# Kernel optimization log

Measured on AMD Instinct MI355X. Metric: run time of the kernel, lower is better.

The kernel has to match this reference:

```python
import jax, jax.numpy as jnp
import numpy as np

V, D, NH, L, E, TOPK, S, B = 512, 768, 12, 4, 8, 2, 1024, 4
DH = int(2.0 * D)  # d_hidden_mult * d_model
DHEAD = D // NH


def setup_inputs() -> dict:
    key = jax.random.key(0)
    ks = jax.random.split(key, 10)
    def n(k, shape):
        return jax.random.normal(k, shape, jnp.float32) * 0.02
    return {
        "x": jax.random.randint(ks[0], (B, S), 0, V),
        "tok_emb": n(ks[1], (V, D)),           # tied with LM head
        "pos_emb": n(ks[2], (1, S, D)),
        "ln1_g": jnp.ones((L, D)), "ln1_b": jnp.zeros((L, D)),
        "qkv_w": n(ks[3], (L, D, 3 * D)), "qkv_b": jnp.zeros((L, 3 * D)),
        "proj_w": n(ks[4], (L, D, D)), "proj_b": jnp.zeros((L, D)),
        "ln2_g": jnp.ones((L, D)), "ln2_b": jnp.zeros((L, D)),
        "gate_w": n(ks[5], (L, D, E)), "gate_b": jnp.zeros((L, E)),
        "w1": n(ks[6], (L, E, D, DH)), "b1": jnp.zeros((L, E, DH)),
        "w2": n(ks[7], (L, E, DH, D)), "b2": jnp.zeros((L, E, D)),
        "lnf_g": jnp.ones((D,)), "lnf_b": jnp.zeros((D,)),
    }


def _layernorm(x, g, b, eps=1e-5):
    m = jnp.mean(x, -1, keepdims=True)
    v = jnp.var(x, -1, keepdims=True)
    return (x - m) / jnp.sqrt(v + eps) * g + b


def _attn(x, qkv_w, qkv_b, proj_w, proj_b):
    b, t, d = x.shape
    qkv = (x @ qkv_w + qkv_b).reshape(b, t, 3, NH, DHEAD)
    qkv = jnp.transpose(qkv, (2, 0, 3, 1, 4))  # [3,B,H,T,dh]
    q, k, v = qkv[0], qkv[1], qkv[2]
    scores = jnp.einsum("bhqd,bhkd->bhqk", q, k) / jnp.sqrt(jnp.float32(DHEAD))
    causal = jnp.tril(jnp.ones((t, t), bool))
    scores = jnp.where(causal[None, None], scores, jnp.finfo(scores.dtype).min)
    attn = jax.nn.softmax(scores, axis=-1)
    out = jnp.einsum("bhqk,bhkd->bhqd", attn, v)
    out = jnp.transpose(out, (0, 2, 1, 3)).reshape(b, t, d)
    return out @ proj_w + proj_b


def _moe(x, gate_w, gate_b, w1, b1, w2, b2):
    b, t, d = x.shape
    xt = x.reshape(-1, d)                                    # [N,D]
    gl = xt @ gate_w + gate_b                                # [N,E]
    probs = jax.nn.softmax(gl, axis=-1)
    topv, topi = jax.lax.top_k(probs, TOPK)                  # [N,K]
    topv = topv / jnp.sum(topv, -1, keepdims=True)           # renormalize top-k
    nidx = jnp.arange(xt.shape[0])[:, None]
    combine = jnp.zeros((xt.shape[0], E), xt.dtype).at[nidx, topi].set(topv)
    h = jax.nn.gelu(jnp.einsum("nd,edh->neh", xt, w1) + b1)  # [N,E,DH]
    eo = jnp.einsum("neh,ehd->ned", h, w2) + b2              # [N,E,D]
    y = jnp.einsum("ne,ned->nd", combine, eo)
    return y.reshape(b, t, d)


def reference(x, tok_emb, pos_emb, ln1_g, ln1_b, qkv_w, qkv_b, proj_w, proj_b,
              ln2_g, ln2_b, gate_w, gate_b, w1, b1, w2, b2, lnf_g, lnf_b):
    h = tok_emb[x] + pos_emb[:, : x.shape[1], :]
    for i in range(L):
        h = h + _attn(_layernorm(h, ln1_g[i], ln1_b[i]), qkv_w[i], qkv_b[i], proj_w[i], proj_b[i])
        h = h + _moe(_layernorm(h, ln2_g[i], ln2_b[i]), gate_w[i], gate_b[i], w1[i], b1[i], w2[i], b2[i])
    h = _layernorm(h, lnf_g, lnf_b)
    logits = h @ tok_emb.T  # tied LM head
    return logits
```

## Files before the change

### kernel.cpp

```cpp
#include <hip/hip_runtime.h>
#include <cstdint>
#include <cstddef>

#define SEQ 1024
#define DMODEL 768
#define NHEAD 12
#define DHEAD 64
#define NLAYER 4
#define NEXP 8
#define DHID 1536
#define VOCAB 512
#define NTOK 4096

typedef __attribute__((ext_vector_type(4))) float f32x4;
typedef __attribute__((ext_vector_type(8))) unsigned short us8v;
typedef __attribute__((ext_vector_type(4))) unsigned short us4v;
typedef __attribute__((ext_vector_type(8))) __bf16 bf16x8;
union FragU { us8v u; bf16x8 b; };

__global__ __launch_bounds__(256) void embed_kernel(const int* __restrict__ x,
    const float* __restrict__ tok, const float* __restrict__ pos, float* __restrict__ h) {
  int i = blockIdx.x * 256 + threadIdx.x;
  int n = i / DMODEL, d = i - n * DMODEL;
  int s = n & (SEQ - 1);
  h[i] = tok[(size_t)x[n] * DMODEL + d] + pos[(size_t)s * DMODEL + d];
}

__global__ __launch_bounds__(256) void ln_kernel(const float* __restrict__ x,
    const float* __restrict__ g, const float* __restrict__ b, float* __restrict__ y) {
  int row = blockIdx.x;
  const float* xr = x + (size_t)row * DMODEL;
  int t = threadIdx.x;
  float v0 = xr[t], v1 = xr[t + 256], v2 = xr[t + 512];
  float s = v0 + v1 + v2;
  float s2 = v0 * v0 + v1 * v1 + v2 * v2;
  for (int off = 32; off; off >>= 1) { s += __shfl_down(s, off); s2 += __shfl_down(s2, off); }
  __shared__ float rs[4], rq[4];
  if ((t & 63) == 0) { rs[t >> 6] = s; rq[t >> 6] = s2; }
  __syncthreads();
  float S  = rs[0] + rs[1] + rs[2] + rs[3];
  float S2 = rq[0] + rq[1] + rq[2] + rq[3];
  float m = S * (1.f / DMODEL);
  float var = S2 * (1.f / DMODEL) - m * m;
  float r = rsqrtf(var + 1e-5f);
  float* yr = y + (size_t)row * DMODEL;
  yr[t]       = (v0 - m) * r * g[t]       + b[t];
  yr[t + 256] = (v1 - m) * r * g[t + 256] + b[t + 256];
  yr[t + 512] = (v2 - m) * r * g[t + 512] + b[t + 512];
}

#define BM 128
#define BN 128
#define BK 32

__device__ __forceinline__ int chx(int row, int kb) {
  return row * 32 + ((kb ^ ((row >> 1) & 3)) << 3);
}

__device__ __forceinline__ void cvt8(const f32x4 x0, const f32x4 x1, us8v& h, us8v& l) {
#pragma unroll
  for (int j = 0; j < 4; j++) {
    unsigned int bb = __float_as_uint(x0[j]);
    h[j] = (unsigned short)(bb >> 16);
    float fl = x0[j] - __uint_as_float(bb & 0xffff0000u);
    l[j] = (unsigned short)(__float_as_uint(fl) >> 16);
  }
#pragma unroll
  for (int j = 0; j < 4; j++) {
    unsigned int bb = __float_as_uint(x1[j]);
    h[4 + j] = (unsigned short)(bb >> 16);
    float fl = x1[j] - __uint_as_float(bb & 0xffff0000u);
    l[4 + j] = (unsigned short)(__float_as_uint(fl) >> 16);
  }
}

template<bool TRANSB, bool RESID>
__global__ __launch_bounds__(256, 2) void gemm_mfma(
    const float* __restrict__ A, const float* __restrict__ Bm,
    const float* __restrict__ bias, float* __restrict__ C,
    int M, int Nn, int K)
{
  __shared__ __align__(16) unsigned short AsH[BM * 32], AsL[BM * 32];
  __shared__ __align__(16) unsigned short BsH[BN * 32], BsL[BN * 32];
  int bm = blockIdx.y * BM, bn = blockIdx.x * BN;
  int tid = threadIdx.x;
  int lane = tid & 63;
  int wid = tid >> 6;
  int wr = wid >> 1, wc = wid & 1;
  int frow = lane & 15, fkb = lane >> 4;
  f32x4 zero = {0.f, 0.f, 0.f, 0.f};
  f32x4 acc[4][4];
#pragma unroll
  for (int i = 0; i < 4; i++)
#pragma unroll
    for (int j = 0; j < 4; j++) acc[i][j] = zero;

  int sr = tid & 127;
  bool doB = tid >= 128;

  for (int k0 = 0; k0 < K; k0 += BK) {
    if (!doB) {
      const float* Ap = A + (size_t)(bm + sr) * K + k0;
#pragma unroll
      for (int c = 0; c < 4; c++) {
        f32x4 x0 = *(const f32x4*)(Ap + c * 8);
        f32x4 x1 = *(const f32x4*)(Ap + c * 8 + 4);
        us8v h, l; cvt8(x0, x1, h, l);
        *(us8v*)&AsH[chx(sr, c)] = h;
        *(us8v*)&AsL[chx(sr, c)] = l;
      }
    } else if (TRANSB) {
      const float* Bp = Bm + (size_t)(bn + sr) * K + k0;
#pragma unroll
      for (int c = 0; c < 4; c++) {
        f32x4 x0 = *(const f32x4*)(Bp + c * 8);
        f32x4 x1 = *(const f32x4*)(Bp + c * 8 + 4);
        us8v h, l; cvt8(x0, x1, h, l);
        *(us8v*)&BsH[chx(sr, c)] = h;
        *(us8v*)&BsL[chx(sr, c)] = l;
      }
    } else {
      const float* Bp = Bm + (size_t)k0 * Nn + bn + sr;
#pragma unroll
      for (int c = 0; c < 4; c++) {
        f32x4 x0, x1;
#pragma unroll
        for (int j = 0; j < 4; j++) x0[j] = Bp[(size_t)(c * 8 + j) * Nn];
#pragma unroll
        for (int j = 0; j < 4; j++) x1[j] = Bp[(size_t)(c * 8 + 4 + j) * Nn];
        us8v h, l; cvt8(x0, x1, h, l);
        *(us8v*)&BsH[chx(sr, c)] = h;
        *(us8v*)&BsL[chx(sr, c)] = l;
      }
    }
    __syncthreads();
    FragU ah[4], al[4], bh[4], bl[4];
#pragma unroll
    for (int i = 0; i < 4; i++) {
      ah[i].u = *(const us8v*)&AsH[chx(wr * 64 + i * 16 + frow, fkb)];
      al[i].u = *(const us8v*)&AsL[chx(wr * 64 + i * 16 + frow, fkb)];
      bh[i].u = *(const us8v*)&BsH[chx(wc * 64 + i * 16 + frow, fkb)];
      bl[i].u = *(const us8v*)&BsL[chx(wc * 64 + i * 16 + frow, fkb)];
    }
#pragma unroll
    for (int i = 0; i < 4; i++)
#pragma unroll
      for (int j = 0; j < 4; j++)
        acc[i][j] = __builtin_amdgcn_mfma_f32_16x16x32_bf16(ah[i].b, bh[j].b, acc[i][j], 0, 0, 0);
#pragma unroll
    for (int i = 0; i < 4; i++)
#pragma unroll
      for (int j = 0; j < 4; j++)
        acc[i][j] = __builtin_amdgcn_mfma_f32_16x16x32_bf16(ah[i].b, bl[j].b, acc[i][j], 0, 0, 0);
#pragma unroll
    for (int i = 0; i < 4; i++)
#pragma unroll
      for (int j = 0; j < 4; j++)
        acc[i][j] = __builtin_amdgcn_mfma_f32_16x16x32_bf16(al[i].b, bh[j].b, acc[i][j], 0, 0, 0);
    __syncthreads();
  }
#pragma unroll
  for (int i = 0; i < 4; i++) {
    int rbase = bm + wr * 64 + i * 16 + (lane >> 4) * 4;
#pragma unroll
    for (int q = 0; q < 4; q++) {
      float* Crow = C + (size_t)(rbase + q) * Nn;
#pragma unroll
      for (int j = 0; j < 4; j++) {
        int col = bn + wc * 64 + j * 16 + frow;
        float v = acc[i][j][q] + (bias ? bias[col] : 0.f);
        if (RESID) v += Crow[col];
        Crow[col] = v;
      }
    }
  }
}

__device__ __forceinline__ float gelu_f(float x) {
  float x3 = x * x * x;
  return 0.5f * x * (1.f + tanhf(0.7978845608028654f * (x + 0.044715f * x3)));
}

template<bool GELU, bool SCALE>
__global__ __launch_bounds__(256, 2) void gemm_moe_mfma(
    const float* __restrict__ A, const float* __restrict__ Bbase,
    const float* __restrict__ biasBase, float* __restrict__ C,
    const int* __restrict__ entries, const int* __restrict__ counts,
    const float* __restrict__ tokw, int Nn, int K)
{
  int e = blockIdx.z;
  int cnt = counts[e];
  int bm = blockIdx.y * BM;
  if (bm >= cnt) return;
  const float* Bm = Bbase + (size_t)e * K * Nn;
  const float* bias = biasBase + (size_t)e * Nn;
  const int* list = entries + e * NTOK;
  int bn = blockIdx.x * BN;
  int tid = threadIdx.x;
  int lane = tid & 63;
  int wid = tid >> 6;
  int wr = wid >> 1, wc = wid & 1;
  int frow = lane & 15, fkb = lane >> 4;

  __shared__ __align__(16) unsigned short AsH[BM * 32], AsL[BM * 32];
  __shared__ __align__(16) unsigned short BsH[BN * 32], BsL[BN * 32];
  __shared__ int rowent[BM];
  if (tid < BM) {
    int gr = bm + tid;
    rowent[tid] = (gr < cnt) ? list[gr] : -1;
  }
  __syncthreads();

  f32x4 zero = {0.f, 0.f, 0.f, 0.f};
  f32x4 acc[4][4];
#pragma unroll
  for (int i = 0; i < 4; i++)
#pragma unroll
    for (int j = 0; j < 4; j++) acc[i][j] = zero;

  int sr = tid & 127;
  bool doB = tid >= 128;

  for (int k0 = 0; k0 < K; k0 += BK) {
    if (!doB) {
      int ent = rowent[sr];
      if (ent >= 0) {
        int arow = GELU ? (ent >> 1) : ent;
        const float* Ap = A + (size_t)arow * K + k0;
#pragma unroll
        for (int c = 0; c < 4; c++) {
          f32x4 x0 = *(const f32x4*)(Ap + c * 8);
          f32x4 x1 = *(const f32x4*)(Ap + c * 8 + 4);
          us8v h, l; cvt8(x0, x1, h, l);
          *(us8v*)&AsH[chx(sr, c)] = h;
          *(us8v*)&AsL[chx(sr, c)] = l;
        }
      } else {
        us8v z = {0, 0, 0, 0, 0, 0, 0, 0};
#pragma unroll
        for (int c = 0; c < 4; c++) {
          *(us8v*)&AsH[chx(sr, c)] = z;
          *(us8v*)&AsL[chx(sr, c)] = z;
        }
      }
    } else {
      const float* Bp = Bm + (size_t)k0 * Nn + bn + sr;
#pragma unroll
      for (int c = 0; c < 4; c++) {
        f32x4 x0, x1;
#pragma unroll
        for (int j = 0; j < 4; j++) x0[j] = Bp[(size_t)(c * 8 + j) * Nn];
#pragma unroll
        for (int j = 0; j < 4; j++) x1[j] = Bp[(size_t)(c * 8 + 4 + j) * Nn];
        us8v h, l; cvt8(x0, x1, h, l);
        *(us8v*)&BsH[chx(sr, c)] = h;
        *(us8v*)&BsL[chx(sr, c)] = l;
      }
    }
    __syncthreads();
    FragU ah[4], al[4], bh[4], bl[4];
#pragma unroll
    for (int i = 0; i < 4; i++) {
      ah[i].u = *(const us8v*)&AsH[chx(wr * 64 + i * 16 + frow, fkb)];
      al[i].u = *(const us8v*)&AsL[chx(wr * 64 + i * 16 + frow, fkb)];
      bh[i].u = *(const us8v*)&BsH[chx(wc * 64 + i * 16 + frow, fkb)];
      bl[i].u = *(const us8v*)&BsL[chx(wc * 64 + i * 16 + frow, fkb)];
    }
#pragma unroll
    for (int i = 0; i < 4; i++)
#pragma unroll
      for (int j = 0; j < 4; j++)
        acc[i][j] = __builtin_amdgcn_mfma_f32_16x16x32_bf16(ah[i].b, bh[j].b, acc[i][j], 0, 0, 0);
#pragma unroll
    for (int i = 0; i < 4; i++)
#pragma unroll
      for (int j = 0; j < 4; j++)
        acc[i][j] = __builtin_amdgcn_mfma_f32_16x16x32_bf16(ah[i].b, bl[j].b, acc[i][j], 0, 0, 0);
#pragma unroll
    for (int i = 0; i < 4; i++)
#pragma unroll
      for (int j = 0; j < 4; j++)
        acc[i][j] = __builtin_amdgcn_mfma_f32_16x16x32_bf16(al[i].b, bh[j].b, acc[i][j], 0, 0, 0);
    __syncthreads();
  }
#pragma unroll
  for (int i = 0; i < 4; i++) {
    int rloc = wr * 64 + i * 16 + (lane >> 4) * 4;
#pragma unroll
    for (int q = 0; q < 4; q++) {
      int ent = rowent[rloc + q];
      if (ent < 0) continue;
      float scl = SCALE ? tokw[ent] : 1.f;
      float* Crow = C + (size_t)ent * Nn;
#pragma unroll
      for (int j = 0; j < 4; j++) {
        int col = bn + wc * 64 + j * 16 + frow;
        float v = acc[i][j][q] + bias[col];
        if (GELU) v = gelu_f(v);
        if (SCALE) v *= scl;
        Crow[col] = v;
      }
    }
  }
}

__device__ __forceinline__ int kvx(int row, int col) {
  return (row << 6) + (((((col >> 3) ^ (row & 7))) << 3) | (col & 7));
}

__global__ __launch_bounds__(256, 2) void fattn_mfma(const float* __restrict__ qkv,
                                                     float* __restrict__ out) {
  int qt = blockIdx.x;
  int hh = blockIdx.y;
  int b  = blockIdx.z;
  int n0 = b * SEQ;
  int q0 = qt * 64;
  const float* base = qkv + (size_t)n0 * (3 * DMODEL);
  int tid = threadIdx.x;
  int lane = tid & 63;
  int w = tid >> 6;
  int fr = lane & 15, fg = lane >> 4;

  __shared__ __align__(16) unsigned short KsH[64 * 64], KsL[64 * 64];
  __shared__ float Vs[64][64];
  __shared__ float Psf[4][16][68];

  FragU qh[2], ql[2];
  {
    const float* qrow = base + (size_t)(q0 + w * 16 + fr) * (3 * DMODEL) + hh * DHEAD;
#pragma unroll
    for (int s = 0; s < 2; s++) {
      f32x4 x0 = *(const f32x4*)(qrow + s * 32 + fg * 8);
      f32x4 x1 = *(const f32x4*)(qrow + s * 32 + fg * 8 + 4);
      x0 *= 0.125f; x1 *= 0.125f;
      cvt8(x0, x1, qh[s].u, ql[s].u);
    }
  }

  f32x4 O[4];
  float m_i[4], l_i[4];
#pragma unroll
  for (int c = 0; c < 4; c++) O[c] = (f32x4){0.f, 0.f, 0.f, 0.f};
#pragma unroll
  for (int r = 0; r < 4; r++) { m_i[r] = -3.4e38f; l_i[r] = 0.f; }

  int krow = tid >> 2, kd = (tid & 3) << 4;

  for (int kt = 0; kt <= qt; kt++) {
    int k0 = kt * 64;
    __syncthreads();
    {
      const float* kp = base + (size_t)(k0 + krow) * (3 * DMODEL) + DMODEL + hh * DHEAD + kd;
      f32x4 x0 = *(const f32x4*)(kp);
      f32x4 x1 = *(const f32x4*)(kp + 4);
      f32x4 x2 = *(const f32x4*)(kp + 8);
      f32x4 x3 = *(const f32x4*)(kp + 12);
      us8v h0, l0, h1, l1;
      cvt8(x0, x1, h0, l0); cvt8(x2, x3, h1, l1);
      *(us8v*)&KsH[kvx(krow, kd)]     = h0;
      *(us8v*)&KsH[kvx(krow, kd + 8)] = h1;
      *(us8v*)&KsL[kvx(krow, kd)]     = l0;
      *(us8v*)&KsL[kvx(krow, kd + 8)] = l1;
    }
    {
#pragma unroll
      for (int it = 0; it < 16; it++) {
        int i = tid + it * 256;
        int r = i >> 6, c = i & 63;
        Vs[r][c] = base[(size_t)(k0 + r) * (3 * DMODEL) + 2 * DMODEL + hh * DHEAD + c];
      }
    }
    __syncthreads();

    f32x4 sa[4];
#pragma unroll
    for (int f = 0; f < 4; f++) sa[f] = (f32x4){0.f, 0.f, 0.f, 0.f};
#pragma unroll
    for (int s = 0; s < 2; s++) {
#pragma unroll
      for (int f = 0; f < 4; f++) {
        FragU kh, kl;
        kh.u = *(const us8v*)&KsH[kvx(f * 16 + fr, s * 32 + fg * 8)];
        kl.u = *(const us8v*)&KsL[kvx(f * 16 + fr, s * 32 + fg * 8)];
        sa[f] = __builtin_amdgcn_mfma_f32_16x16x32_bf16(qh[s].b, kh.b, sa[f], 0, 0, 0);
        sa[f] = __builtin_amdgcn_mfma_f32_16x16x32_bf16(qh[s].b, kl.b, sa[f], 0, 0, 0);
        sa[f] = __builtin_amdgcn_mfma_f32_16x16x32_bf16(ql[s].b, kh.b, sa[f], 0, 0, 0);
      }
    }
    if (kt == qt) {
#pragma unroll
      for (int f = 0; f < 4; f++)
#pragma unroll
        for (int r = 0; r < 4; r++)
          if (k0 + f * 16 + fr > q0 + w * 16 + fg * 4 + r) sa[f][r] = -3.4e38f;
    }

#pragma unroll
    for (int r = 0; r < 4; r++) {
      float rm = fmaxf(fmaxf(sa[0][r], sa[1][r]), fmaxf(sa[2][r], sa[3][r]));
      rm = fmaxf(rm, __shfl_xor(rm, 1));
      rm = fmaxf(rm, __shfl_xor(rm, 2));
      rm = fmaxf(rm, __shfl_xor(rm, 4));
      rm = fmaxf(rm, __shfl_xor(rm, 8));
      float mnew = fmaxf(m_i[r], rm);
      float alpha = __expf(m_i[r] - mnew);
      m_i[r] = mnew;
      float rsum = 0.f;
#pragma unroll
      for (int f = 0; f < 4; f++) {
        float p = __expf(sa[f][r] - mnew);
        rsum += p;
        Psf[w][fg * 4 + r][f * 16 + fr] = p;
      }
      rsum += __shfl_xor(rsum, 1);
      rsum += __shfl_xor(rsum, 2);
      rsum += __shfl_xor(rsum, 4);
      rsum += __shfl_xor(rsum, 8);
      l_i[r] = l_i[r] * alpha + rsum;
#pragma unroll
      for (int c = 0; c < 4; c++) O[c][r] *= alpha;
    }
    __syncthreads();

    for (int kk = 0; kk < 64; kk++) {
      float pr[4], vv[4];
#pragma unroll
      for (int r = 0; r < 4; r++) pr[r] = Psf[w][fg * 4 + r][kk];
#pragma unroll
      for (int c = 0; c < 4; c++) vv[c] = Vs[kk][c * 16 + fr];
#pragma unroll
      for (int c = 0; c < 4; c++)
#pragma unroll
        for (int r = 0; r < 4; r++) O[c][r] += pr[r] * vv[c];
    }
  }

#pragma unroll
  for (int r = 0; r < 4; r++) {
    float rinv = 1.f / l_i[r];
    float* orow = out + (size_t)(n0 + q0 + w * 16 + fg * 4 + r) * DMODEL + hh * DHEAD;
#pragma unroll
    for (int c = 0; c < 4; c++) orow[c * 16 + fr] = O[c][r] * rinv;
  }
}

__global__ __launch_bounds__(256) void gate_kernel(const float* __restrict__ xln,
    const float* __restrict__ gw, const float* __restrict__ gb,
    int* __restrict__ counts, int* __restrict__ entries, float* __restrict__ tokw) {
  int n = blockIdx.x * 256 + threadIdx.x;
  if (n >= NTOK) return;
  const float* xr = xln + (size_t)n * DMODEL;
  float gl[NEXP];
#pragma unroll
  for (int e = 0; e < NEXP; e++) gl[e] = gb[e];
  for (int dd = 0; dd < DMODEL; dd++) {
    float xv = xr[dd];
#pragma unroll
    for (int e = 0; e < NEXP; e++) gl[e] += xv * gw[dd * NEXP + e];
  }
  float mx = gl[0];
#pragma unroll
  for (int e = 1; e < NEXP; e++) mx = fmaxf(mx, gl[e]);
  float ex[NEXP];
#pragma unroll
  for (int e = 0; e < NEXP; e++) ex[e] = expf(gl[e] - mx);
  int i0 = 0; float v0 = ex[0];
#pragma unroll
  for (int e = 1; e < NEXP; e++) if (ex[e] > v0) { v0 = ex[e]; i0 = e; }
  int i1 = -1; float v1 = -1.f;
#pragma unroll
  for (int e = 0; e < NEXP; e++) if (e != i0 && ex[e] > v1) { v1 = ex[e]; i1 = e; }
  float wsum = v0 + v1;
  float w0 = v0 / wsum, w1 = v1 / wsum;
  int p0 = atomicAdd(&counts[i0], 1);
  entries[i0 * NTOK + p0] = n * 2 + 0;
  tokw[n * 2 + 0] = w0;
  int p1 = atomicAdd(&counts[i1], 1);
  entries[i1 * NTOK + p1] = n * 2 + 1;
  tokw[n * 2 + 1] = w1;
}

__global__ void zero_counts(int* c) { if (threadIdx.x < NEXP) c[threadIdx.x] = 0; }

__global__ __launch_bounds__(256) void combine_kernel(float* __restrict__ h,
                                                      const float* __restrict__ eo) {
  int i = blockIdx.x * 256 + threadIdx.x;
  int n = i / DMODEL, d = i - n * DMODEL;
  h[i] += eo[(size_t)(n * 2) * DMODEL + d] + eo[(size_t)(n * 2 + 1) * DMODEL + d];
}

extern "C" void kernel_launch(void* const* d_in, const int* in_sizes, int n_in,
                              void* d_out, int out_size, void* d_ws, size_t ws_size,
                              hipStream_t stream) {
  const int*   x       = (const int*)d_in[0];
  const float* tok_emb = (const float*)d_in[1];
  const float* pos_emb = (const float*)d_in[2];
  const float* ln1_g   = (const float*)d_in[3];
  const float* ln1_b   = (const float*)d_in[4];
  const float* qkv_w   = (const float*)d_in[5];
  const float* qkv_b   = (const float*)d_in[6];
  const float* proj_w  = (const float*)d_in[7];
  const float* proj_b  = (const float*)d_in[8];
  const float* ln2_g   = (const float*)d_in[9];
  const float* ln2_b   = (const float*)d_in[10];
  const float* gate_w  = (const float*)d_in[11];
  const float* gate_b  = (const float*)d_in[12];
  const float* w1      = (const float*)d_in[13];
  const float* b1      = (const float*)d_in[14];
  const float* w2      = (const float*)d_in[15];
  const float* b2      = (const float*)d_in[16];
  const float* lnf_g   = (const float*)d_in[17];
  const float* lnf_b   = (const float*)d_in[18];
  float* out = (float*)d_out;

  const size_t ND = (size_t)NTOK * DMODEL;
  float* h    = (float*)d_ws;
  float* xln  = h + ND;
  float* R    = xln + ND;
  float* R2   = R + (size_t)2 * NTOK * DHID;
  float* tokw = R2 + (size_t)2 * NTOK * DMODEL;
  int* counts  = (int*)(tokw + 2 * NTOK);
  int* entries = counts + NEXP;

  float* qkvbuf   = R;
  float* H1       = R;
  float* attn_out = R2;
  float* eo       = R2;

  dim3 blk(256);
  embed_kernel<<<ND / 256, blk, 0, stream>>>(x, tok_emb, pos_emb, h);
  for (int l = 0; l < NLAYER; l++) {
    ln_kernel<<<NTOK, blk, 0, stream>>>(h, ln1_g + l * DMODEL, ln1_b + l * DMODEL, xln);
    gemm_mfma<false, false><<<dim3(3 * DMODEL / BN, NTOK / BM), blk, 0, stream>>>(
        xln, qkv_w + (size_t)l * DMODEL * 3 * DMODEL, qkv_b + l * 3 * DMODEL,
        qkvbuf, NTOK, 3 * DMODEL, DMODEL);
    fattn_mfma<<<dim3(SEQ / 64, NHEAD, 4), blk, 0, stream>>>(qkvbuf, attn_out);
    gemm_mfma<false, true><<<dim3(DMODEL / BN, NTOK / BM), blk, 0, stream>>>(
        attn_out, proj_w + (size_t)l * DMODEL * DMODEL, proj_b + l * DMODEL,
        h, NTOK, DMODEL, DMODEL);
    ln_kernel<<<NTOK, blk, 0, stream>>>(h, ln2_g + l * DMODEL, ln2_b + l * DMODEL, xln);
    zero_counts<<<1, 64, 0, stream>>>(counts);
    gate_kernel<<<NTOK / 256, blk, 0, stream>>>(
        xln, gate_w + (size_t)l * DMODEL * NEXP, gate_b + l * NEXP, counts, entries, tokw);
    gemm_moe_mfma<true, false><<<dim3(DHID / BN, NTOK / BM, NEXP), blk, 0, stream>>>(
        xln, w1 + (size_t)l * NEXP * DMODEL * DHID, b1 + (size_t)l * NEXP * DHID,
        H1, entries, counts, tokw, DHID, DMODEL);
    gemm_moe_mfma<false, true><<<dim3(DMODEL / BN, NTOK / BM, NEXP), blk, 0, stream>>>(
        H1, w2 + (size_t)l * NEXP * DHID * DMODEL, b2 + (size_t)l * NEXP * DMODEL,
        eo, entries, counts, tokw, DMODEL, DHID);
    combine_kernel<<<ND / 256, blk, 0, stream>>>(h, eo);
  }
  ln_kernel<<<NTOK, blk, 0, stream>>>(h, lnf_g, lnf_b, xln);
  gemm_mfma<true, false><<<dim3(VOCAB / BN, NTOK / BM), blk, 0, stream>>>(
      xln, tok_emb, nullptr, out, NTOK, VOCAB, DMODEL);
}
```

Baseline: 3.374 ms.

## Pre-split operands into bf16 hi/lo planes and transpose weights before GEMMs

Weights are converted once per layer into transposed bf16 hi/lo arrays by a new split-transpose kernel. Activations are emitted already split by layernorm, attention and the first MoE GEMM. The GEMM inner loops then copy ready-made u16 data instead of loading fp32, splitting, and doing strided column reads of untransposed B. This removes redundant conversion work and uncoalesced B loads, at the cost of extra per-call weight preprocessing passes and a larger workspace.

```diff
diff --git a/kernel.cpp b/kernel.cpp
--- a/kernel.cpp
+++ b/kernel.cpp
@@ -17,6 +17,27 @@
 typedef __attribute__((ext_vector_type(4))) unsigned short us4v;
 typedef __attribute__((ext_vector_type(8))) __bf16 bf16x8;
 union FragU { us8v u; bf16x8 b; };
+typedef unsigned short u16;
+
+__device__ __forceinline__ void split1(float x, u16& h, u16& l) {
+  unsigned int u = __float_as_uint(x);
+  h = (u16)(u >> 16);
+  float fl = x - __uint_as_float(u & 0xffff0000u);
+  l = (u16)(__float_as_uint(fl) >> 16);
+}
+
+__device__ __forceinline__ void cvt8(const f32x4 x0, const f32x4 x1, us8v& h, us8v& l) {
+#pragma unroll
+  for (int j = 0; j < 4; j++) { u16 hh, ll; split1(x0[j], hh, ll); h[j] = hh; l[j] = ll; }
+#pragma unroll
+  for (int j = 0; j < 4; j++) { u16 hh, ll; split1(x1[j], hh, ll); h[4 + j] = hh; l[4 + j] = ll; }
+}
+
+__device__ __forceinline__ void cvt4(float a, float b, float c, float d, us4v& h, us4v& l) {
+  float x[4] = {a, b, c, d};
+#pragma unroll
+  for (int j = 0; j < 4; j++) { u16 hh, ll; split1(x[j], hh, ll); h[j] = hh; l[j] = ll; }
+}
 
 __global__ __launch_bounds__(256) void embed_kernel(const int* __restrict__ x,
     const float* __restrict__ tok, const float* __restrict__ pos, float* __restrict__ h) {
@@ -27,7 +48,8 @@
 }
 
 __global__ __launch_bounds__(256) void ln_kernel(const float* __restrict__ x,
-    const float* __restrict__ g, const float* __restrict__ b, float* __restrict__ y) {
+    const float* __restrict__ g, const float* __restrict__ b, float* __restrict__ y,
+    u16* __restrict__ yh, u16* __restrict__ yl) {
   int row = blockIdx.x;
   const float* xr = x + (size_t)row * DMODEL;
   int t = threadIdx.x;
@@ -43,10 +65,56 @@
   float m = S * (1.f / DMODEL);
   float var = S2 * (1.f / DMODEL) - m * m;
   float r = rsqrtf(var + 1e-5f);
-  float* yr = y + (size_t)row * DMODEL;
-  yr[t]       = (v0 - m) * r * g[t]       + b[t];
-  yr[t + 256] = (v1 - m) * r * g[t + 256] + b[t + 256];
-  yr[t + 512] = (v2 - m) * r * g[t + 512] + b[t + 512];
+  size_t base = (size_t)row * DMODEL;
+#pragma unroll
+  for (int q = 0; q < 3; q++) {
+    int idx = t + q * 256;
+    float v = (q == 0 ? v0 : (q == 1 ? v1 : v2));
+    float o = (v - m) * r * g[idx] + b[idx];
+    y[base + idx] = o;
+    u16 hh, ll; split1(o, hh, ll);
+    yh[base + idx] = hh; yl[base + idx] = ll;
+  }
+}
+
+__global__ __launch_bounds__(256) void split_tr_kernel(const float* __restrict__ src,
+    u16* __restrict__ dh, u16* __restrict__ dl, int K, int N) {
+  size_t slab = (size_t)blockIdx.z * K * N;
+  src += slab; dh += slab; dl += slab;
+  int n0 = blockIdx.x * 64, k0 = blockIdx.y * 64;
+  __shared__ u16 Th[64][72], Tl[64][72];
+  int t = threadIdx.x;
+  int vk = (t >> 4) * 4;
+  int vn = (t & 15) * 4;
+  const float* sp = src + (size_t)(k0 + vk) * N + n0 + vn;
+  f32x4 r0 = *(const f32x4*)(sp);
+  f32x4 r1 = *(const f32x4*)(sp + N);
+  f32x4 r2 = *(const f32x4*)(sp + 2 * N);
+  f32x4 r3 = *(const f32x4*)(sp + 3 * N);
+#pragma unroll
+  for (int j = 0; j < 4; j++) {
+    us4v hh, ll;
+    cvt4(r0[j], r1[j], r2[j], r3[j], hh, ll);
+    *(us4v*)&Th[vn + j][vk] = hh;
+    *(us4v*)&Tl[vn + j][vk] = ll;
+  }
+  __syncthreads();
+  int nr = t >> 2, kc = (t & 3) * 16;
+  u16* dhp = dh + (size_t)(n0 + nr) * K + k0 + kc;
+  u16* dlp = dl + (size_t)(n0 + nr) * K + k0 + kc;
+  *(us8v*)dhp       = *(const us8v*)&Th[nr][kc];
+  *(us8v*)(dhp + 8) = *(const us8v*)&Th[nr][kc + 8];
+  *(us8v*)dlp       = *(const us8v*)&Tl[nr][kc];
+  *(us8v*)(dlp + 8) = *(const us8v*)&Tl[nr][kc + 8];
+}
+
+__global__ __launch_bounds__(256) void split_copy_kernel(const float* __restrict__ src,
+    u16* __restrict__ dh, u16* __restrict__ dl) {
+  int i = (blockIdx.x * 256 + threadIdx.x) * 8;
+  f32x4 x0 = *(const f32x4*)(src + i);
+  f32x4 x1 = *(const f32x4*)(src + i + 4);
+  us8v h, l; cvt8(x0, x1, h, l);
+  *(us8v*)&dh[i] = h; *(us8v*)&dl[i] = l;
 }
 
 #define BM 128
@@ -57,31 +125,15 @@
   return row * 32 + ((kb ^ ((row >> 1) & 3)) << 3);
 }
 
-__device__ __forceinline__ void cvt8(const f32x4 x0, const f32x4 x1, us8v& h, us8v& l) {
-#pragma unroll
-  for (int j = 0; j < 4; j++) {
-    unsigned int bb = __float_as_uint(x0[j]);
-    h[j] = (unsigned short)(bb >> 16);
-    float fl = x0[j] - __uint_as_float(bb & 0xffff0000u);
-    l[j] = (unsigned short)(__float_as_uint(fl) >> 16);
-  }
-#pragma unroll
-  for (int j = 0; j < 4; j++) {
-    unsigned int bb = __float_as_uint(x1[j]);
-    h[4 + j] = (unsigned short)(bb >> 16);
-    float fl = x1[j] - __uint_as_float(bb & 0xffff0000u);
-    l[4 + j] = (unsigned short)(__float_as_uint(fl) >> 16);
-  }
-}
-
-template<bool TRANSB, bool RESID>
-__global__ __launch_bounds__(256, 2) void gemm_mfma(
-    const float* __restrict__ A, const float* __restrict__ Bm,
+template<bool RESID>
+__global__ __launch_bounds__(256, 2) void gemm_mfma_s(
+    const u16* __restrict__ Ah, const u16* __restrict__ Al,
+    const u16* __restrict__ Bh, const u16* __restrict__ Bl,
     const float* __restrict__ bias, float* __restrict__ C,
-    int M, int Nn, int K)
+    int Nn, int K)
 {
-  __shared__ __align__(16) unsigned short AsH[BM * 32], AsL[BM * 32];
-  __shared__ __align__(16) unsigned short BsH[BN * 32], BsL[BN * 32];
+  __shared__ __align__(16) u16 AsH[BM * 32], AsL[BM * 32];
+  __shared__ __align__(16) u16 BsH[BN * 32], BsL[BN * 32];
   int bm = blockIdx.y * BM, bn = blockIdx.x * BN;
   int tid = threadIdx.x;
   int lane = tid & 63;
@@ -100,37 +152,20 @@
 
   for (int k0 = 0; k0 < K; k0 += BK) {
     if (!doB) {
-      const float* Ap = A + (size_t)(bm + sr) * K + k0;
+      const u16* ph = Ah + (size_t)(bm + sr) * K + k0;
+      const u16* pl = Al + (size_t)(bm + sr) * K + k0;
 #pragma unroll
       for (int c = 0; c < 4; c++) {
-        f32x4 x0 = *(const f32x4*)(Ap + c * 8);
-        f32x4 x1 = *(const f32x4*)(Ap + c * 8 + 4);
-        us8v h, l; cvt8(x0, x1, h, l);
-        *(us8v*)&AsH[chx(sr, c)] = h;
-        *(us8v*)&AsL[chx(sr, c)] = l;
-      }
-    } else if (TRANSB) {
-      const float* Bp = Bm + (size_t)(bn + sr) * K + k0;
+        *(us8v*)&AsH[chx(sr, c)] = *(const us8v*)(ph + c * 8);
+        *(us8v*)&AsL[chx(sr, c)] = *(const us8v*)(pl + c * 8);
+      }
+    } else {
+      const u16* ph = Bh + (size_t)(bn + sr) * K + k0;
+      const u16* pl = Bl + (size_t)(bn + sr) * K + k0;
 #pragma unroll
       for (int c = 0; c < 4; c++) {
-        f32x4 x0 = *(const f32x4*)(Bp + c * 8);
-        f32x4 x1 = *(const f32x4*)(Bp + c * 8 + 4);
-        us8v h, l; cvt8(x0, x1, h, l);
-        *(us8v*)&BsH[chx(sr, c)] = h;
-        *(us8v*)&BsL[chx(sr, c)] = l;
-      }
-    } else {
-      const float* Bp = Bm + (size_t)k0 * Nn + bn + sr;
-#pragma unroll
-      for (int c = 0; c < 4; c++) {
-        f32x4 x0, x1;
-#pragma unroll
-        for (int j = 0; j < 4; j++) x0[j] = Bp[(size_t)(c * 8 + j) * Nn];
-#pragma unroll
-        for (int j = 0; j < 4; j++) x1[j] = Bp[(size_t)(c * 8 + 4 + j) * Nn];
-        us8v h, l; cvt8(x0, x1, h, l);
-        *(us8v*)&BsH[chx(sr, c)] = h;
-        *(us8v*)&BsL[chx(sr, c)] = l;
+        *(us8v*)&BsH[chx(sr, c)] = *(const us8v*)(ph + c * 8);
+        *(us8v*)&BsL[chx(sr, c)] = *(const us8v*)(pl + c * 8);
       }
     }
     __syncthreads();
@@ -181,10 +216,12 @@
   return 0.5f * x * (1.f + tanhf(0.7978845608028654f * (x + 0.044715f * x3)));
 }
 
-template<bool GELU, bool SCALE>
-__global__ __launch_bounds__(256, 2) void gemm_moe_mfma(
-    const float* __restrict__ A, const float* __restrict__ Bbase,
-    const float* __restrict__ biasBase, float* __restrict__ C,
+template<bool GELU>
+__global__ __launch_bounds__(256, 2) void gemm_moe_mfma_s(
+    const u16* __restrict__ Ah, const u16* __restrict__ Al,
+    const u16* __restrict__ Bh, const u16* __restrict__ Bl,
+    const float* __restrict__ biasBase,
+    float* __restrict__ Cf, u16* __restrict__ Ch, u16* __restrict__ Cl,
     const int* __restrict__ entries, const int* __restrict__ counts,
     const float* __restrict__ tokw, int Nn, int K)
 {
@@ -192,7 +229,8 @@
   int cnt = counts[e];
   int bm = blockIdx.y * BM;
   if (bm >= cnt) return;
-  const float* Bm = Bbase + (size_t)e * K * Nn;
+  const u16* Bph = Bh + (size_t)e * K * Nn;
+  const u16* Bpl = Bl + (size_t)e * K * Nn;
   const float* bias = biasBase + (size_t)e * Nn;
   const int* list = entries + e * NTOK;
   int bn = blockIdx.x * BN;
@@ -202,8 +240,8 @@
   int wr = wid >> 1, wc = wid & 1;
   int frow = lane & 15, fkb = lane >> 4;
 
-  __shared__ __align__(16) unsigned short AsH[BM * 32], AsL[BM * 32];
-  __shared__ __align__(16) unsigned short BsH[BN * 32], BsL[BN * 32];
+  __shared__ __align__(16) u16 AsH[BM * 32], AsL[BM * 32];
+  __shared__ __align__(16) u16 BsH[BN * 32], BsL[BN * 32];
   __shared__ int rowent[BM];
   if (tid < BM) {
     int gr = bm + tid;
@@ -226,14 +264,12 @@
       int ent = rowent[sr];
       if (ent >= 0) {
         int arow = GELU ? (ent >> 1) : ent;
-        const float* Ap = A + (size_t)arow * K + k0;
+        const u16* ph = Ah + (size_t)arow * K + k0;
+        const u16* pl = Al + (size_t)arow * K + k0;
 #pragma unroll
         for (int c = 0; c < 4; c++) {
-          f32x4 x0 = *(const f32x4*)(Ap + c * 8);
-          f32x4 x1 = *(const f32x4*)(Ap + c * 8 + 4);
-          us8v h, l; cvt8(x0, x1, h, l);
-          *(us8v*)&AsH[chx(sr, c)] = h;
-          *(us8v*)&AsL[chx(sr, c)] = l;
+          *(us8v*)&AsH[chx(sr, c)] = *(const us8v*)(ph + c * 8);
+          *(us8v*)&AsL[chx(sr, c)] = *(const us8v*)(pl + c * 8);
         }
       } else {
         us8v z = {0, 0, 0, 0, 0, 0, 0, 0};
@@ -244,17 +280,12 @@
         }
       }
     } else {
-      const float* Bp = Bm + (size_t)k0 * Nn + bn + sr;
+      const u16* ph = Bph + (size_t)(bn + sr) * K + k0;
+      const u16* pl = Bpl + (size_t)(bn + sr) * K + k0;
 #pragma unroll
       for (int c = 0; c < 4; c++) {
-        f32x4 x0, x1;
-#pragma unroll
-        for (int j = 0; j < 4; j++) x0[j] = Bp[(size_t)(c * 8 + j) * Nn];
-#pragma unroll
-        for (int j = 0; j < 4; j++) x1[j] = Bp[(size_t)(c * 8 + 4 + j) * Nn];
-        us8v h, l; cvt8(x0, x1, h, l);
-        *(us8v*)&BsH[chx(sr, c)] = h;
-        *(us8v*)&BsL[chx(sr, c)] = l;
+        *(us8v*)&BsH[chx(sr, c)] = *(const us8v*)(ph + c * 8);
+        *(us8v*)&BsL[chx(sr, c)] = *(const us8v*)(pl + c * 8);
       }
     }
     __syncthreads();
@@ -290,15 +321,18 @@
     for (int q = 0; q < 4; q++) {
       int ent = rowent[rloc + q];
       if (ent < 0) continue;
-      float scl = SCALE ? tokw[ent] : 1.f;
-      float* Crow = C + (size_t)ent * Nn;
 #pragma unroll
       for (int j = 0; j < 4; j++) {
         int col = bn + wc * 64 + j * 16 + frow;
         float v = acc[i][j][q] + bias[col];
-        if (GELU) v = gelu_f(v);
-        if (SCALE) v *= scl;
-        Crow[col] = v;
+        if (GELU) {
+          v = gelu_f(v);
+          u16 hh, ll; split1(v, hh, ll);
+          Ch[(size_t)ent * Nn + col] = hh;
+          Cl[(size_t)ent * Nn + col] = ll;
+        } else {
+          Cf[(size_t)ent * Nn + col] = v * tokw[ent];
+        }
       }
     }
   }
@@ -309,7 +343,8 @@
 }
 
 __global__ __launch_bounds__(256, 2) void fattn_mfma(const float* __restrict__ qkv,
-                                                     float* __restrict__ out) {
+                                                     u16* __restrict__ outh,
+                                                     u16* __restrict__ outl) {
   int qt = blockIdx.x;
   int hh = blockIdx.y;
   int b  = blockIdx.z;
@@ -321,7 +356,7 @@
   int w = tid >> 6;
   int fr = lane & 15, fg = lane >> 4;
 
-  __shared__ __align__(16) unsigned short KsH[64 * 64], KsL[64 * 64];
+  __shared__ __align__(16) u16 KsH[64 * 64], KsL[64 * 64];
   __shared__ float Vs[64][64];
   __shared__ float Psf[4][16][68];
 
@@ -438,9 +473,14 @@
 #pragma unroll
   for (int r = 0; r < 4; r++) {
     float rinv = 1.f / l_i[r];
-    float* orow = out + (size_t)(n0 + q0 + w * 16 + fg * 4 + r) * DMODEL + hh * DHEAD;
-#pragma unroll
-    for (int c = 0; c < 4; c++) orow[c * 16 + fr] = O[c][r] * rinv;
+    size_t obase = (size_t)(n0 + q0 + w * 16 + fg * 4 + r) * DMODEL + hh * DHEAD;
+#pragma unroll
+    for (int c = 0; c < 4; c++) {
+      float o = O[c][r] * rinv;
+      u16 hh2, ll2; split1(o, hh2, ll2);
+      outh[obase + c * 16 + fr] = hh2;
+      outl[obase + c * 16 + fr] = ll2;
+    }
   }
 }
 
@@ -514,43 +554,63 @@
   float* out = (float*)d_out;
 
   const size_t ND = (size_t)NTOK * DMODEL;
-  float* h    = (float*)d_ws;
-  float* xln  = h + ND;
-  float* R    = xln + ND;
-  float* R2   = R + (size_t)2 * NTOK * DHID;
-  float* tokw = R2 + (size_t)2 * NTOK * DMODEL;
-  int* counts  = (int*)(tokw + 2 * NTOK);
-  int* entries = counts + NEXP;
-
-  float* qkvbuf   = R;
-  float* H1       = R;
-  float* attn_out = R2;
-  float* eo       = R2;
+  char* W = (char*)d_ws;
+  float* h      = (float*)W;  W += ND * 4;
+  float* xln    = (float*)W;  W += ND * 4;
+  u16*   xh     = (u16*)W;    W += ND * 2;
+  u16*   xl     = (u16*)W;    W += ND * 2;
+  float* qkvbuf = (float*)W;  W += 3 * ND * 4;
+  u16*   aoh    = (u16*)W;    W += ND * 2;
+  u16*   aol    = (u16*)W;    W += ND * 2;
+  u16*   H1h    = (u16*)W;    W += (size_t)2 * NTOK * DHID * 2;
+  u16*   H1l    = (u16*)W;    W += (size_t)2 * NTOK * DHID * 2;
+  float* eo     = (float*)W;  W += (size_t)2 * NTOK * DMODEL * 4;
+  float* tokw   = (float*)W;  W += 2 * NTOK * 4;
+  int*   counts = (int*)W;    W += 32;
+  int*   entries= (int*)W;    W += (size_t)NEXP * NTOK * 4;
+  u16*   WTqh   = (u16*)W;    W += (size_t)DMODEL * 3 * DMODEL * 2;
+  u16*   WTql   = (u16*)W;    W += (size_t)DMODEL * 3 * DMODEL * 2;
+  u16*   WTph   = (u16*)W;    W += (size_t)DMODEL * DMODEL * 2;
+  u16*   WTpl   = (u16*)W;    W += (size_t)DMODEL * DMODEL * 2;
+  u16*   WT1h   = (u16*)W;    W += (size_t)NEXP * DMODEL * DHID * 2;
+  u16*   WT1l   = (u16*)W;    W += (size_t)NEXP * DMODEL * DHID * 2;
+  u16*   WT2h   = (u16*)W;    W += (size_t)NEXP * DHID * DMODEL * 2;
+  u16*   WT2l   = (u16*)W;    W += (size_t)NEXP * DHID * DMODEL * 2;
 
   dim3 blk(256);
   embed_kernel<<<ND / 256, blk, 0, stream>>>(x, tok_emb, pos_emb, h);
   for (int l = 0; l < NLAYER; l++) {
-    ln_kernel<<<NTOK, blk, 0, stream>>>(h, ln1_g + l * DMODEL, ln1_b + l * DMODEL, xln);
-    gemm_mfma<false, false><<<dim3(3 * DMODEL / BN, NTOK / BM), blk, 0, stream>>>(
-        xln, qkv_w + (size_t)l * DMODEL * 3 * DMODEL, qkv_b + l * 3 * DMODEL,
-        qkvbuf, NTOK, 3 * DMODEL, DMODEL);
-    fattn_mfma<<<dim3(SEQ / 64, NHEAD, 4), blk, 0, stream>>>(qkvbuf, attn_out);
-    gemm_mfma<false, true><<<dim3(DMODEL / BN, NTOK / BM), blk, 0, stream>>>(
-        attn_out, proj_w + (size_t)l * DMODEL * DMODEL, proj_b + l * DMODEL,
-        h, NTOK, DMODEL, DMODEL);
-    ln_kernel<<<NTOK, blk, 0, stream>>>(h, ln2_g + l * DMODEL, ln2_b + l * DMODEL, xln);
+    split_tr_kernel<<<dim3(3 * DMODEL / 64, DMODEL / 64, 1), blk, 0, stream>>>(
+        qkv_w + (size_t)l * DMODEL * 3 * DMODEL, WTqh, WTql, DMODEL, 3 * DMODEL);
+    split_tr_kernel<<<dim3(DMODEL / 64, DMODEL / 64, 1), blk, 0, stream>>>(
+        proj_w + (size_t)l * DMODEL * DMODEL, WTph, WTpl, DMODEL, DMODEL);
+    split_tr_kernel<<<dim3(DHID / 64, DMODEL / 64, NEXP), blk, 0, stream>>>(
+        w1 + (size_t)l * NEXP * DMODEL * DHID, WT1h, WT1l, DMODEL, DHID);
+    split_tr_kernel<<<dim3(DMODEL / 64, DHID / 64, NEXP), blk, 0, stream>>>(
+        w2 + (size_t)l * NEXP * DHID * DMODEL, WT2h, WT2l, DHID, DMODEL);
+
+    ln_kernel<<<NTOK, blk, 0, stream>>>(h, ln1_g + l * DMODEL, ln1_b + l * DMODEL,
+                                        xln, xh, xl);
+    gemm_mfma_s<false><<<dim3(3 * DMODEL / BN, NTOK / BM), blk, 0, stream>>>(
+        xh, xl, WTqh, WTql, qkv_b + l * 3 * DMODEL, qkvbuf, 3 * DMODEL, DMODEL);
+    fattn_mfma<<<dim3(SEQ / 64, NHEAD, 4), blk, 0, stream>>>(qkvbuf, aoh, aol);
+    gemm_mfma_s<true><<<dim3(DMODEL / BN, NTOK / BM), blk, 0, stream>>>(
+        aoh, aol, WTph, WTpl, proj_b + l * DMODEL, h, DMODEL, DMODEL);
+    ln_kernel<<<NTOK, blk, 0, stream>>>(h, ln2_g + l * DMODEL, ln2_b + l * DMODEL,
+                                        xln, xh, xl);
     zero_counts<<<1, 64, 0, stream>>>(counts);
     gate_kernel<<<NTOK / 256, blk, 0, stream>>>(
         xln, gate_w + (size_t)l * DMODEL * NEXP, gate_b + l * NEXP, counts, entries, tokw);
-    gemm_moe_mfma<true, false><<<dim3(DHID / BN, NTOK / BM, NEXP), blk, 0, stream>>>(
-        xln, w1 + (size_t)l * NEXP * DMODEL * DHID, b1 + (size_t)l * NEXP * DHID,
-        H1, entries, counts, tokw, DHID, DMODEL);
-    gemm_moe_mfma<false, true><<<dim3(DMODEL / BN, NTOK / BM, NEXP), blk, 0, stream>>>(
-        H1, w2 + (size_t)l * NEXP * DHID * DMODEL, b2 + (size_t)l * NEXP * DMODEL,
-        eo, entries, counts, tokw, DMODEL, DHID);
+    gemm_moe_mfma_s<true><<<dim3(DHID / BN, NTOK / BM, NEXP), blk, 0, stream>>>(
+        xh, xl, WT1h, WT1l, b1 + (size_t)l * NEXP * DHID,
+        nullptr, H1h, H1l, entries, counts, tokw, DHID, DMODEL);
+    gemm_moe_mfma_s<false><<<dim3(DMODEL / BN, NTOK / BM, NEXP), blk, 0, stream>>>(
+        H1h, H1l, WT2h, WT2l, b2 + (size_t)l * NEXP * DMODEL,
+        eo, nullptr, nullptr, entries, counts, tokw, DMODEL, DHID);
     combine_kernel<<<ND / 256, blk, 0, stream>>>(h, eo);
   }
-  ln_kernel<<<NTOK, blk, 0, stream>>>(h, lnf_g, lnf_b, xln);
-  gemm_mfma<true, false><<<dim3(VOCAB / BN, NTOK / BM), blk, 0, stream>>>(
-      xln, tok_emb, nullptr, out, NTOK, VOCAB, DMODEL);
-}
+  ln_kernel<<<NTOK, blk, 0, stream>>>(h, lnf_g, lnf_b, xln, xh, xl);
+  split_copy_kernel<<<(VOCAB * DMODEL) / (256 * 8), blk, 0, stream>>>(tok_emb, WTqh, WTql);
+  gemm_mfma_s<false><<<dim3(VOCAB / BN, NTOK / BM), blk, 0, stream>>>(
+      xh, xl, WTqh, WTql, nullptr, out, VOCAB, DMODEL);
+}
```

New measurement: 4.121 ms. +22.1%, slower.
